# Optimization experiments

Hardware: AMD Instinct MI355X
Metric: run time of the kernel (lower is better)

## Reference

```python
import jax, jax.numpy as jnp
import numpy as np

B, N, C = 4, 2048, 768
H = 6  # 3 obj heads + 3 pose heads (forced by the chained matmul shapes)


def setup_inputs() -> dict:
    key = jax.random.key(0)
    k1, k2, k3 = jax.random.split(key, 3)
    x = jax.random.normal(k1, (B, N, C), dtype=jnp.float32)
    w_qkv = jax.random.normal(k2, (3 * C, C), dtype=jnp.float32) * (C ** -0.5)
    w_proj = jax.random.normal(k3, (C, C // 2), dtype=jnp.float32) * ((C // 2) ** -0.5)
    b_proj = jnp.zeros((C,), dtype=jnp.float32)
    return {"x": x, "w_qkv": w_qkv, "w_proj": w_proj, "b_proj": b_proj, "num_heads": H}


def reference(x, w_qkv, w_proj, b_proj, num_heads):
    b, n, c = x.shape
    hd = c // num_heads
    scale = hd ** -0.5
    # qkv projection -> [3, B, H, N, hd]
    qkv = (x @ w_qkv.T).reshape(b, n, 3, num_heads, hd)
    qkv = jnp.transpose(qkv, (2, 0, 3, 1, 4))
    q, k, v = qkv[0], qkv[1], qkv[2]
    # head split: first 3 heads -> obj (sigmoid), last 3 -> pose (softmax)
    attn_obj = jax.nn.sigmoid(jnp.einsum('bhqd,bhkd->bhqk', q[:, 0:3], k[:, 0:3]) * scale)
    attn_pose = jax.nn.softmax(jnp.einsum('bhqd,bhkd->bhqk', q[:, 3:], k[:, 3:]) * scale, axis=-1)
    # chained matmuls: (attn_pose @ (attn_obj @ v_pose))  -> [B, 3, N, hd]
    ctx = jnp.einsum('bhqk,bhkd->bhqd', attn_obj, v[:, 3:])
    ctx = jnp.einsum('bhqk,bhkd->bhqd', attn_pose, ctx)
    out = jnp.transpose(ctx, (0, 2, 1, 3)).reshape(b, n, c // 2)
    out = out @ w_proj.T + b_proj
    return out, attn_obj
```

## Files before the change

kernel.cpp:

```cpp
#include <hip/hip_runtime.h>

typedef _Float16 half8 __attribute__((ext_vector_type(8)));
typedef _Float16 half4v __attribute__((ext_vector_type(4)));
typedef float f32x4 __attribute__((ext_vector_type(4)));
typedef float f32x16 __attribute__((ext_vector_type(16)));

#define MFMA16(a, b, c) __builtin_amdgcn_mfma_f32_16x16x32_f16((a), (b), (c), 0, 0, 0)
#define MFMA32(a, b, c) __builtin_amdgcn_mfma_f32_32x32x16_f16((a), (b), (c), 0, 0, 0)
#define FENCE() __builtin_amdgcn_sched_barrier(0)
#define BAR() __builtin_amdgcn_s_barrier()

__device__ __forceinline__ void gl_lds16(const void* g, void* l) {
  __builtin_amdgcn_global_load_lds(
      (const __attribute__((address_space(1))) unsigned int*)g,
      (__attribute__((address_space(3))) unsigned int*)l, 16, 0, 0);
}

__device__ __forceinline__ unsigned pkh2(float a, float b) {
  unsigned lo = (unsigned)__builtin_bit_cast(unsigned short, (_Float16)a);
  unsigned hf = (unsigned)__builtin_bit_cast(unsigned short, (_Float16)b);
  return lo | (hf << 16);
}

__global__ __launch_bounds__(256) void k_cvt_all(const float* __restrict__ x,
                                                 const float* __restrict__ wq,
                                                 const float* __restrict__ wp,
                                                 _Float16* __restrict__ xb,
                                                 _Float16* __restrict__ wqb,
                                                 _Float16* __restrict__ wpb) {
  int i = blockIdx.x * 256 + threadIdx.x;
  const float4* src;
  half4v* dst;
  int j;
  if (i < 1572864) { src = (const float4*)x; dst = (half4v*)xb; j = i; }
  else if (i < 1572864 + 442368) { src = (const float4*)wq; dst = (half4v*)wqb; j = i - 1572864; }
  else if (i < 2088960) { src = (const float4*)wp; dst = (half4v*)wpb; j = i - 2015232; }
  else return;
  float4 v = src[j];
  half4v h;
  h[0] = (_Float16)v.x; h[1] = (_Float16)v.y;
  h[2] = (_Float16)v.z; h[3] = (_Float16)v.w;
  dst[j] = h;
}

__global__ __launch_bounds__(256) void k_qkv(const _Float16* __restrict__ A,
                                             const _Float16* __restrict__ Bt,
                                             _Float16* __restrict__ Qw,
                                             _Float16* __restrict__ Kw,
                                             _Float16* __restrict__ Vtw) {
  __shared__ _Float16 As[2][128 * 32];
  __shared__ _Float16 Bs[2][128 * 32];
  const int tid = threadIdx.x;
  const int w = tid >> 6, l = tid & 63;
  const int wr = w >> 1, wc = w & 1;
  const int bid0 = blockIdx.x;
  const int bid = (bid0 & 7) * 144 + (bid0 >> 3);
  const int tm = bid / 18, tn = bid % 18;
  const int m0 = tm * 128, n0 = tn * 128;

  auto stage = [&](int it, int dst) {
    int k0 = it * 32;
#pragma unroll
    for (int r = 0; r < 2; ++r) {
      int seg = r * 256 + tid;
      int row = seg >> 2, cs = seg & 3;
      gl_lds16(A + (size_t)(m0 + row) * 768 + k0 + cs * 8, (char*)As[dst] + (r * 256 + w * 64) * 16);
      gl_lds16(Bt + (size_t)(n0 + row) * 768 + k0 + cs * 8, (char*)Bs[dst] + (r * 256 + w * 64) * 16);
    }
  };

  f32x4 acc[4][4] = {};
  stage(0, 0);
  asm volatile("s_waitcnt vmcnt(0)" ::: "memory");
  BAR();
  for (int it = 0; it < 24; ++it) {
    const int cur = it & 1;
    stage(it < 23 ? it + 1 : 23, cur ^ 1);
    asm volatile("s_waitcnt vmcnt(4)" ::: "memory");
    FENCE();
    BAR();
    FENCE();
#pragma unroll
    for (int m = 0; m < 4; ++m) {
      half8 av = *(const half8*)&As[cur][(wr * 64 + m * 16 + (l & 15)) * 32 + (l >> 4) * 8];
#pragma unroll
      for (int n = 0; n < 4; ++n) {
        half8 bv = *(const half8*)&Bs[cur][(wc * 64 + n * 16 + (l & 15)) * 32 + (l >> 4) * 8];
        acc[m][n] = MFMA16(av, bv, acc[m][n]);
      }
    }
    FENCE();
    BAR();
  }
  asm volatile("s_waitcnt vmcnt(0)" ::: "memory");

  const float scale = 0.08838834764831845f;
#pragma unroll
  for (int m = 0; m < 4; ++m) {
    int gmb = m0 + wr * 64 + m * 16 + ((l >> 4) << 2);
#pragma unroll
    for (int n = 0; n < 4; ++n) {
      int gn0 = n0 + wc * 64 + n * 16;
      int t = gn0 / 768, rem = gn0 % 768;
      int h = rem >> 7, d = (rem & 127) + (l & 15);
      if (t == 2) {
        int bB = gmb >> 11, ntok0 = gmb & 2047;
        half4v hv;
#pragma unroll
        for (int j = 0; j < 4; ++j) hv[j] = (_Float16)acc[m][n][j];
        *(half4v*)&Vtw[((size_t)(bB * 6 + h) * 128 + d) * 2048 + ntok0] = hv;
      } else {
#pragma unroll
        for (int j = 0; j < 4; ++j) {
          int gm = gmb + j;
          int b = gm >> 11, ntok = gm & 2047;
          float v = acc[m][n][j];
          if (t == 0)
            Qw[((size_t)(b * 6 + h) * 2048 + ntok) * 128 + d] = (_Float16)(v * scale);
          else
            Kw[((size_t)(b * 6 + h) * 2048 + ntok) * 128 + d] = (_Float16)v;
        }
      }
    }
  }
}

__global__ __launch_bounds__(256, 3) void k_obj(const _Float16* __restrict__ Qw,
                                                const _Float16* __restrict__ Kw,
                                                const _Float16* __restrict__ Vtw,
                                                float* __restrict__ attn,
                                                float* __restrict__ c1p) {
  __shared__ _Float16 Ks[2][64 * 128];
  __shared__ _Float16 Vs[128 * 64];
  __shared__ float Ts[4][256];
  const int tid = threadIdx.x, w = tid >> 6, l = tid & 63;
  const int wr = w >> 1, wc = w & 1, hi = l >> 5, q = l & 31;
  const int bid0 = blockIdx.x;
  const int bid = (bid0 & 7) * 96 + (bid0 >> 3);
  const int kvh = bid & 1, u = bid >> 1;
  const int b = u / 96, remu = u % 96, h = remu / 32, qb = remu % 32;
  const int kvbase = kvh * 1024;
  const _Float16* Qg = Qw + ((size_t)(b * 6 + h) * 2048 + qb * 64 + wr * 32) * 128;
  const _Float16* Kg = Kw + ((size_t)(b * 6 + h) * 2048 + kvbase) * 128;
  const _Float16* Vg = Vtw + ((size_t)(b * 6 + h + 3) * 128) * 2048 + kvbase;
  float* attng = attn + ((size_t)(b * 3 + h) * 2048 + qb * 64) * 2048 + kvbase;
  float* c1g = c1p + ((size_t)(kvh * 12 + b * 3 + h) * 128) * 2048;

  auto stageK = [&](int t, int dstb) {
#pragma unroll
    for (int r = 0; r < 4; ++r) {
      int seg = r * 256 + tid;
      int row = seg >> 4, cs = (seg & 15) ^ (row & 7);
      gl_lds16(Kg + (size_t)(t * 64 + row) * 128 + cs * 8,
               (char*)Ks[dstb] + (r * 256 + w * 64) * 16);
    }
  };
  auto stageV = [&](int t) {
#pragma unroll
    for (int r = 0; r < 4; ++r) {
      int seg = r * 256 + tid;
      int row = seg >> 3, cs = (seg & 7) ^ (row & 7);
      gl_lds16(Vg + (size_t)row * 2048 + t * 64 + cs * 8,
               (char*)Vs + (r * 256 + w * 64) * 16);
    }
  };

  half8 qreg[8];
#pragma unroll
  for (int s = 0; s < 8; ++s)
    qreg[s] = *(const half8*)&Qg[(size_t)q * 128 + s * 16 + hi * 8];
  stageK(0, 0);

  f32x16 acc[4] = {};
  for (int kt = 0; kt < 16; ++kt) {
    const int cur = kt & 1, nxt = cur ^ 1;
    stageV(kt);
    stageK((kt + 1) & 15, nxt);
    asm volatile("s_waitcnt vmcnt(8)" ::: "memory");
    FENCE(); BAR(); FENCE();
    f32x16 p = {};
    const int krow = wc * 32 + q;
    __builtin_amdgcn_s_setprio(1);
#pragma unroll
    for (int s = 0; s < 8; ++s) {
      int chunk = (s * 2 + hi) ^ (krow & 7);
      half8 av = *(const half8*)&Ks[cur][krow * 128 + chunk * 8];
      p = MFMA32(av, qreg[s], p);
    }
    __builtin_amdgcn_s_setprio(0);
#pragma unroll
    for (int r = 0; r < 16; ++r) p[r] = 1.0f / (1.0f + __expf(-p[r]));
    union { unsigned uu[4]; half8 v; } bf0, bf1;
    {
      unsigned pk01 = pkh2(p[0], p[1]), pk23 = pkh2(p[2], p[3]);
      unsigned pk45 = pkh2(p[4], p[5]), pk67 = pkh2(p[6], p[7]);
      unsigned x = hi ? pk01 : pk45, y = hi ? pk23 : pk67;
      unsigned xsw = (unsigned)__shfl_xor((int)x, 32);
      unsigned ysw = (unsigned)__shfl_xor((int)y, 32);
      bf0.uu[0] = hi ? xsw : pk01; bf0.uu[1] = hi ? ysw : pk23;
      bf0.uu[2] = hi ? pk45 : xsw; bf0.uu[3] = hi ? pk67 : ysw;
    }
    {
      unsigned pk01 = pkh2(p[8], p[9]), pk23 = pkh2(p[10], p[11]);
      unsigned pk45 = pkh2(p[12], p[13]), pk67 = pkh2(p[14], p[15]);
      unsigned x = hi ? pk01 : pk45, y = hi ? pk23 : pk67;
      unsigned xsw = (unsigned)__shfl_xor((int)x, 32);
      unsigned ysw = (unsigned)__shfl_xor((int)y, 32);
      bf1.uu[0] = hi ? xsw : pk01; bf1.uu[1] = hi ? ysw : pk23;
      bf1.uu[2] = hi ? pk45 : xsw; bf1.uu[3] = hi ? pk67 : ysw;
    }
    asm volatile("s_waitcnt vmcnt(4)" ::: "memory");
    FENCE(); BAR(); FENCE();
    __builtin_amdgcn_s_setprio(1);
#pragma unroll
    for (int ks = 0; ks < 2; ++ks) {
#pragma unroll
      for (int dt = 0; dt < 4; ++dt) {
        int vrow = dt * 32 + q;
        int chunk = (wc * 4 + ks * 2 + hi) ^ (vrow & 7);
        half8 av = *(const half8*)&Vs[vrow * 64 + chunk * 8];
        acc[dt] = MFMA32(av, ks ? bf1.v : bf0.v, acc[dt]);
      }
    }
    __builtin_amdgcn_s_setprio(0);
#pragma unroll
    for (int rho = 0; rho < 4; ++rho) {
      asm volatile("s_waitcnt lgkmcnt(0)" ::: "memory");
      FENCE();
      if ((q >> 3) == rho) {
        int qr = q & 7;
#pragma unroll
        for (int g = 0; g < 4; ++g) {
          f32x4 vv;
          vv[0] = p[g * 4 + 0]; vv[1] = p[g * 4 + 1];
          vv[2] = p[g * 4 + 2]; vv[3] = p[g * 4 + 3];
          int kv0 = g * 8 + hi * 4;
          *(f32x4*)&Ts[w][qr * 32 + (kv0 ^ (qr << 2))] = vv;
        }
      }
      asm volatile("s_waitcnt lgkmcnt(0)" ::: "memory");
      FENCE();
      {
        int row = l >> 3, c0 = (l & 7) * 4;
        f32x4 vv = *(const f32x4*)&Ts[w][row * 32 + (c0 ^ (row << 2))];
        *(f32x4*)&attng[(size_t)(wr * 32 + rho * 8 + row) * 2048 + kt * 64 + wc * 32 + c0] = vv;
      }
    }
    FENCE();
    BAR();
  }
  __syncthreads();
  float* mb = (float*)Ks;
  if (wc == 1) {
#pragma unroll
    for (int dt = 0; dt < 4; ++dt)
#pragma unroll
      for (int r = 0; r < 16; ++r) {
        int d = dt * 32 + (r & 3) + 8 * (r >> 2) + 4 * hi;
        mb[(wr * 128 + d) * 32 + q] = acc[dt][r];
      }
  }
  __syncthreads();
  if (wc == 0) {
    int n = qb * 64 + wr * 32 + q;
#pragma unroll
    for (int dt = 0; dt < 4; ++dt)
#pragma unroll
      for (int r = 0; r < 16; ++r) {
        int d = dt * 32 + (r & 3) + 8 * (r >> 2) + 4 * hi;
        c1g[(size_t)d * 2048 + n] = acc[dt][r] + mb[(wr * 128 + d) * 32 + q];
      }
  }
}

__global__ __launch_bounds__(256) void k_merge1(const float* __restrict__ c1p,
                                                _Float16* __restrict__ c1t) {
  int i = blockIdx.x * 256 + threadIdx.x;
  f32x4 a = ((const f32x4*)c1p)[i];
  f32x4 bb = ((const f32x4*)c1p)[i + 786432];
  half4v hv;
#pragma unroll
  for (int j = 0; j < 4; ++j) hv[j] = (_Float16)(a[j] + bb[j]);
  ((half4v*)c1t)[i] = hv;
}

__global__ __launch_bounds__(256, 3) void k_pose(const _Float16* __restrict__ Qw,
                                                 const _Float16* __restrict__ Kw,
                                                 const _Float16* __restrict__ c1t,
                                                 float* __restrict__ p2,
                                                 float* __restrict__ lsumw) {
  __shared__ _Float16 Ks[2][64 * 128];
  __shared__ _Float16 Cs[128 * 64];
  __shared__ float lbuf[64];
  const int tid = threadIdx.x, w = tid >> 6, l = tid & 63;
  const int wr = w >> 1, wc = w & 1, hi = l >> 5, q = l & 31;
  const int bid0 = blockIdx.x;
  const int bid = (bid0 & 7) * 96 + (bid0 >> 3);
  const int kvh = bid & 1, u = bid >> 1;
  const int b = u / 96, remu = u % 96, h = remu / 32, qb = remu % 32;
  const int kvbase = kvh * 1024;
  const _Float16* Qg = Qw + ((size_t)(b * 6 + h + 3) * 2048 + qb * 64 + wr * 32) * 128;
  const _Float16* Kg = Kw + ((size_t)(b * 6 + h + 3) * 2048 + kvbase) * 128;
  const _Float16* Cg = c1t + ((size_t)(b * 3 + h) * 128) * 2048 + kvbase;
  float* p2g = p2 + (size_t)kvh * 3145728 + (size_t)b * 2048 * 384;

  auto stageK = [&](int t, int dstb) {
#pragma unroll
    for (int r = 0; r < 4; ++r) {
      int seg = r * 256 + tid;
      int row = seg >> 4, cs = (seg & 15) ^ (row & 7);
      gl_lds16(Kg + (size_t)(t * 64 + row) * 128 + cs * 8,
               (char*)Ks[dstb] + (r * 256 + w * 64) * 16);
    }
  };
  auto stageC = [&](int t) {
#pragma unroll
    for (int r = 0; r < 4; ++r) {
      int seg = r * 256 + tid;
      int row = seg >> 3, cs = (seg & 7) ^ (row & 7);
      gl_lds16(Cg + (size_t)row * 2048 + t * 64 + cs * 8,
               (char*)Cs + (r * 256 + w * 64) * 16);
    }
  };

  half8 qreg[8];
#pragma unroll
  for (int s = 0; s < 8; ++s)
    qreg[s] = *(const half8*)&Qg[(size_t)q * 128 + s * 16 + hi * 8];
  stageK(0, 0);

  f32x16 acc[4] = {};
  float lsum = 0.f;
  for (int kt = 0; kt < 16; ++kt) {
    const int cur = kt & 1, nxt = cur ^ 1;
    stageC(kt);
    stageK((kt + 1) & 15, nxt);
    asm volatile("s_waitcnt vmcnt(8)" ::: "memory");
    FENCE(); BAR(); FENCE();
    f32x16 p = {};
    const int krow = wc * 32 + q;
    __builtin_amdgcn_s_setprio(1);
#pragma unroll
    for (int s = 0; s < 8; ++s) {
      int chunk = (s * 2 + hi) ^ (krow & 7);
      half8 av = *(const half8*)&Ks[cur][krow * 128 + chunk * 8];
      p = MFMA32(av, qreg[s], p);
    }
    __builtin_amdgcn_s_setprio(0);
#pragma unroll
    for (int r = 0; r < 16; ++r) {
      p[r] = __expf(p[r]);
      lsum += p[r];
    }
    union { unsigned uu[4]; half8 v; } bf0, bf1;
    {
      unsigned pk01 = pkh2(p[0], p[1]), pk23 = pkh2(p[2], p[3]);
      unsigned pk45 = pkh2(p[4], p[5]), pk67 = pkh2(p[6], p[7]);
      unsigned x = hi ? pk01 : pk45, y = hi ? pk23 : pk67;
      unsigned xsw = (unsigned)__shfl_xor((int)x, 32);
      unsigned ysw = (unsigned)__shfl_xor((int)y, 32);
      bf0.uu[0] = hi ? xsw : pk01; bf0.uu[1] = hi ? ysw : pk23;
      bf0.uu[2] = hi ? pk45 : xsw; bf0.uu[3] = hi ? pk67 : ysw;
    }
    {
      unsigned pk01 = pkh2(p[8], p[9]), pk23 = pkh2(p[10], p[11]);
      unsigned pk45 = pkh2(p[12], p[13]), pk67 = pkh2(p[14], p[15]);
      unsigned x = hi ? pk01 : pk45, y = hi ? pk23 : pk67;
      unsigned xsw = (unsigned)__shfl_xor((int)x, 32);
      unsigned ysw = (unsigned)__shfl_xor((int)y, 32);
      bf1.uu[0] = hi ? xsw : pk01; bf1.uu[1] = hi ? ysw : pk23;
      bf1.uu[2] = hi ? pk45 : xsw; bf1.uu[3] = hi ? pk67 : ysw;
    }
    asm volatile("s_waitcnt vmcnt(4)" ::: "memory");
    FENCE(); BAR(); FENCE();
    __builtin_amdgcn_s_setprio(1);
#pragma unroll
    for (int ks = 0; ks < 2; ++ks) {
#pragma unroll
      for (int dt = 0; dt < 4; ++dt) {
        int vrow = dt * 32 + q;
        int chunk = (wc * 4 + ks * 2 + hi) ^ (vrow & 7);
        half8 av = *(const half8*)&Cs[vrow * 64 + chunk * 8];
        acc[dt] = MFMA32(av, ks ? bf1.v : bf0.v, acc[dt]);
      }
    }
    __builtin_amdgcn_s_setprio(0);
    FENCE();
    BAR();
  }
  __syncthreads();
  float lsum2 = lsum + (float)__shfl_xor(lsum, 32);
  float* mb = (float*)Ks;
  if (wc == 1) {
#pragma unroll
    for (int dt = 0; dt < 4; ++dt)
#pragma unroll
      for (int r = 0; r < 16; ++r) {
        int d = dt * 32 + (r & 3) + 8 * (r >> 2) + 4 * hi;
        mb[(wr * 128 + d) * 32 + q] = acc[dt][r];
      }
    if (hi == 0) lbuf[wr * 32 + q] = lsum2;
  }
  __syncthreads();
  float* Cf = (float*)Cs;
  if (wc == 0) {
#pragma unroll
    for (int dt = 0; dt < 4; ++dt)
#pragma unroll
      for (int r = 0; r < 16; ++r) {
        int d = dt * 32 + (r & 3) + 8 * (r >> 2) + 4 * hi;
        acc[dt][r] += mb[(wr * 128 + d) * 32 + q];
      }
    float lsump = lsum2 + lbuf[wr * 32 + q];
    if (hi == 0)
      lsumw[(size_t)(kvh * 12 + b * 3 + h) * 2048 + qb * 64 + wr * 32 + q] = lsump;
  }
#pragma unroll
  for (int rr = 0; rr < 2; ++rr) {
    __syncthreads();
    if (wc == 0 && wr == rr) {
#pragma unroll
      for (int dt = 0; dt < 4; ++dt)
#pragma unroll
        for (int g = 0; g < 4; ++g) {
          int d0 = dt * 32 + g * 8 + hi * 4, c = d0 >> 2;
          f32x4 vv;
          vv[0] = acc[dt][g * 4 + 0]; vv[1] = acc[dt][g * 4 + 1];
          vv[2] = acc[dt][g * 4 + 2]; vv[3] = acc[dt][g * 4 + 3];
          *(f32x4*)&Cf[q * 128 + ((c ^ ((q & 7) << 2)) << 2)] = vv;
        }
    }
    __syncthreads();
    {
      int nl = tid >> 3, cbase = (tid & 7) * 4;
#pragma unroll
      for (int j = 0; j < 4; ++j) {
        int c = cbase + j;
        f32x4 vv = *(const f32x4*)&Cf[nl * 128 + ((c ^ ((nl & 7) << 2)) << 2)];
        *(f32x4*)&p2g[(size_t)(qb * 64 + rr * 32 + nl) * 384 + h * 128 + (c << 2)] = vv;
      }
    }
  }
}

__global__ __launch_bounds__(256) void k_merge2(const float* __restrict__ p2,
                                                const float* __restrict__ lsumw,
                                                _Float16* __restrict__ c2) {
  int i = blockIdx.x * 256 + threadIdx.x;
  size_t i4 = (size_t)i * 4;
  int n = (int)(i4 / 384);
  int h = ((int)(i4 % 384)) >> 7;
  int b = n >> 11, nl = n & 2047;
  int hh = b * 3 + h;
  float ls = lsumw[hh * 2048 + nl] + lsumw[24576 + hh * 2048 + nl];
  float inv = 1.0f / ls;
  f32x4 a = ((const f32x4*)p2)[i];
  f32x4 bb = ((const f32x4*)p2)[i + 786432];
  half4v hv;
#pragma unroll
  for (int j = 0; j < 4; ++j) hv[j] = (_Float16)((a[j] + bb[j]) * inv);
  ((half4v*)c2)[i] = hv;
}

__global__ __launch_bounds__(256) void k_proj(const _Float16* __restrict__ A,
                                              const _Float16* __restrict__ Bt,
                                              const float* __restrict__ bias,
                                              float* __restrict__ out) {
  __shared__ _Float16 As[2][128 * 32];
  __shared__ _Float16 Bs[2][128 * 32];
  const int tid = threadIdx.x;
  const int w = tid >> 6, l = tid & 63;
  const int wr = w >> 1, wc = w & 1;
  const int bid0 = blockIdx.x;
  const int bid = (bid0 & 7) * 48 + (bid0 >> 3);
  const int tm = bid / 6, tn = bid % 6;
  const int m0 = tm * 128, n0 = tn * 128;

  auto stage = [&](int it, int dst) {
    int k0 = it * 32;
#pragma unroll
    for (int r = 0; r < 2; ++r) {
      int seg = r * 256 + tid;
      int row = seg >> 2, cs = seg & 3;
      gl_lds16(A + (size_t)(m0 + row) * 384 + k0 + cs * 8, (char*)As[dst] + (r * 256 + w * 64) * 16);
      gl_lds16(Bt + (size_t)(n0 + row) * 384 + k0 + cs * 8, (char*)Bs[dst] + (r * 256 + w * 64) * 16);
    }
  };

  f32x4 acc[4][4] = {};
  stage(0, 0);
  asm volatile("s_waitcnt vmcnt(0)" ::: "memory");
  BAR();
  for (int it = 0; it < 12; ++it) {
    const int cur = it & 1;
    stage(it < 11 ? it + 1 : 11, cur ^ 1);
    asm volatile("s_waitcnt vmcnt(4)" ::: "memory");
    FENCE();
    BAR();
    FENCE();
#pragma unroll
    for (int m = 0; m < 4; ++m) {
      half8 av = *(const half8*)&As[cur][(wr * 64 + m * 16 + (l & 15)) * 32 + (l >> 4) * 8];
#pragma unroll
      for (int n = 0; n < 4; ++n) {
        half8 bv = *(const half8*)&Bs[cur][(wc * 64 + n * 16 + (l & 15)) * 32 + (l >> 4) * 8];
        acc[m][n] = MFMA16(av, bv, acc[m][n]);
      }
    }
    FENCE();
    BAR();
  }
  asm volatile("s_waitcnt vmcnt(0)" ::: "memory");

#pragma unroll
  for (int m = 0; m < 4; ++m) {
    int gmb = m0 + wr * 64 + m * 16 + ((l >> 4) << 2);
#pragma unroll
    for (int n = 0; n < 4; ++n) {
      int gn = n0 + wc * 64 + n * 16 + (l & 15);
      float bv = bias[gn];
#pragma unroll
      for (int j = 0; j < 4; ++j) {
        int gm = gmb + j;
        out[(size_t)gm * 768 + gn] = acc[m][n][j] + bv;
      }
    }
  }
}

extern "C" void kernel_launch(void* const* d_in, const int* in_sizes, int n_in,
                              void* d_out, int out_size, void* d_ws, size_t ws_size,
                              hipStream_t stream) {
  const float* x = (const float*)d_in[0];
  const float* wqkv = (const float*)d_in[1];
  const float* wproj = (const float*)d_in[2];
  const float* bproj = (const float*)d_in[3];

  _Float16* xb = (_Float16*)d_ws;
  _Float16* wqkvb = xb + 6291456;
  _Float16* wprojb = wqkvb + 1769472;
  _Float16* Qw = wprojb + 294912;
  _Float16* Kw = Qw + 6291456;
  _Float16* Vtw = Kw + 6291456;
  _Float16* c1t = Vtw + 6291456;
  _Float16* c2 = c1t + 3145728;
  float* c1p = (float*)(c2 + 3145728);
  float* p2 = c1p + 6291456;
  float* lsumw = p2 + 6291456;

  float* out = (float*)d_out;
  float* attn = out + 6291456;

  k_cvt_all<<<8160, 256, 0, stream>>>(x, wqkv, wproj, xb, wqkvb, wprojb);
  k_qkv<<<1152, 256, 0, stream>>>(xb, wqkvb, Qw, Kw, Vtw);
  k_obj<<<768, 256, 0, stream>>>(Qw, Kw, Vtw, attn, c1p);
  k_merge1<<<3072, 256, 0, stream>>>(c1p, c1t);
  k_pose<<<768, 256, 0, stream>>>(Qw, Kw, c1t, p2, lsumw);
  k_merge2<<<3072, 256, 0, stream>>>(p2, lsumw, c2);
  k_proj<<<384, 256, 0, stream>>>(c2, wprojb, bproj, out);
}
```

Before: 216.7 us.

## Remove split-KV in obj/pose kernels and fuse merges into epilogues

The obj and pose attention kernels no longer split the key range into two halves. Each block now loops over all 2048 keys and writes the final fp16 context directly, normalised by the softmax sum in the pose case. This removes the two merge kernels and the fp32 partial buffers, along with their global traffic and launch cost. The attn tile store is reorganised to do a single LDS transpose per tile, and occupancy for k_obj drops to 2 blocks per CU. The trade-off is half as many blocks (384 on a 256-CU device), which risks poor load balance and less latency hiding.

```diff
diff --git a/kernel.cpp b/kernel.cpp
--- a/kernel.cpp
+++ b/kernel.cpp
@@ -125,26 +125,23 @@
   }
 }
 
-__global__ __launch_bounds__(256, 3) void k_obj(const _Float16* __restrict__ Qw,
+__global__ __launch_bounds__(256, 2) void k_obj(const _Float16* __restrict__ Qw,
                                                 const _Float16* __restrict__ Kw,
                                                 const _Float16* __restrict__ Vtw,
                                                 float* __restrict__ attn,
-                                                float* __restrict__ c1p) {
+                                                _Float16* __restrict__ c1t) {
   __shared__ _Float16 Ks[2][64 * 128];
   __shared__ _Float16 Vs[128 * 64];
-  __shared__ float Ts[4][256];
+  __shared__ float Ts[4][1024];
   const int tid = threadIdx.x, w = tid >> 6, l = tid & 63;
   const int wr = w >> 1, wc = w & 1, hi = l >> 5, q = l & 31;
   const int bid0 = blockIdx.x;
-  const int bid = (bid0 & 7) * 96 + (bid0 >> 3);
-  const int kvh = bid & 1, u = bid >> 1;
-  const int b = u / 96, remu = u % 96, h = remu / 32, qb = remu % 32;
-  const int kvbase = kvh * 1024;
+  const int bid = (bid0 & 7) * 48 + (bid0 >> 3);
+  const int b = bid / 96, rem = bid % 96, h = rem / 32, qb = rem % 32;
   const _Float16* Qg = Qw + ((size_t)(b * 6 + h) * 2048 + qb * 64 + wr * 32) * 128;
-  const _Float16* Kg = Kw + ((size_t)(b * 6 + h) * 2048 + kvbase) * 128;
-  const _Float16* Vg = Vtw + ((size_t)(b * 6 + h + 3) * 128) * 2048 + kvbase;
-  float* attng = attn + ((size_t)(b * 3 + h) * 2048 + qb * 64) * 2048 + kvbase;
-  float* c1g = c1p + ((size_t)(kvh * 12 + b * 3 + h) * 128) * 2048;
+  const _Float16* Kg = Kw + ((size_t)(b * 6 + h) * 2048) * 128;
+  const _Float16* Vg = Vtw + ((size_t)(b * 6 + h + 3) * 128) * 2048;
+  float* attng = attn + ((size_t)(b * 3 + h) * 2048 + qb * 64) * 2048;
 
   auto stageK = [&](int t, int dstb) {
 #pragma unroll
@@ -172,10 +169,10 @@
   stageK(0, 0);
 
   f32x16 acc[4] = {};
-  for (int kt = 0; kt < 16; ++kt) {
+  for (int kt = 0; kt < 32; ++kt) {
     const int cur = kt & 1, nxt = cur ^ 1;
     stageV(kt);
-    stageK((kt + 1) & 15, nxt);
+    stageK((kt + 1) & 31, nxt);
     asm volatile("s_waitcnt vmcnt(8)" ::: "memory");
     FENCE(); BAR(); FENCE();
     f32x16 p = {};
@@ -223,27 +220,19 @@
       }
     }
     __builtin_amdgcn_s_setprio(0);
-#pragma unroll
-    for (int rho = 0; rho < 4; ++rho) {
-      asm volatile("s_waitcnt lgkmcnt(0)" ::: "memory");
-      FENCE();
-      if ((q >> 3) == rho) {
-        int qr = q & 7;
-#pragma unroll
-        for (int g = 0; g < 4; ++g) {
-          f32x4 vv;
-          vv[0] = p[g * 4 + 0]; vv[1] = p[g * 4 + 1];
-          vv[2] = p[g * 4 + 2]; vv[3] = p[g * 4 + 3];
-          int kv0 = g * 8 + hi * 4;
-          *(f32x4*)&Ts[w][qr * 32 + (kv0 ^ (qr << 2))] = vv;
-        }
-      }
-      asm volatile("s_waitcnt lgkmcnt(0)" ::: "memory");
-      FENCE();
-      {
-        int row = l >> 3, c0 = (l & 7) * 4;
-        f32x4 vv = *(const f32x4*)&Ts[w][row * 32 + (c0 ^ (row << 2))];
-        *(f32x4*)&attng[(size_t)(wr * 32 + rho * 8 + row) * 2048 + kt * 64 + wc * 32 + c0] = vv;
+    {
+      float* T = Ts[w];
+#pragma unroll
+      for (int r = 0; r < 16; ++r) {
+        int kv = (r & 3) + 8 * (r >> 2) + 4 * hi;
+        T[q * 32 + (kv ^ ((q & 7) << 2))] = p[r];
+      }
+#pragma unroll
+      for (int i = 0; i < 4; ++i) {
+        int qr = (l >> 3) + 8 * i;
+        int kvq = (l & 7) * 4;
+        f32x4 v4 = *(const f32x4*)&T[qr * 32 + (kvq ^ ((qr & 7) << 2))];
+        *(f32x4*)&attng[(size_t)(wr * 32 + qr) * 2048 + kt * 64 + wc * 32 + kvq] = v4;
       }
     }
     FENCE();
@@ -262,47 +251,33 @@
   }
   __syncthreads();
   if (wc == 0) {
+    _Float16* cg = c1t + (size_t)(b * 3 + h) * 128 * 2048;
     int n = qb * 64 + wr * 32 + q;
 #pragma unroll
     for (int dt = 0; dt < 4; ++dt)
 #pragma unroll
       for (int r = 0; r < 16; ++r) {
         int d = dt * 32 + (r & 3) + 8 * (r >> 2) + 4 * hi;
-        c1g[(size_t)d * 2048 + n] = acc[dt][r] + mb[(wr * 128 + d) * 32 + q];
-      }
-  }
-}
-
-__global__ __launch_bounds__(256) void k_merge1(const float* __restrict__ c1p,
-                                                _Float16* __restrict__ c1t) {
-  int i = blockIdx.x * 256 + threadIdx.x;
-  f32x4 a = ((const f32x4*)c1p)[i];
-  f32x4 bb = ((const f32x4*)c1p)[i + 786432];
-  half4v hv;
-#pragma unroll
-  for (int j = 0; j < 4; ++j) hv[j] = (_Float16)(a[j] + bb[j]);
-  ((half4v*)c1t)[i] = hv;
+        cg[(size_t)d * 2048 + n] = (_Float16)(acc[dt][r] + mb[(wr * 128 + d) * 32 + q]);
+      }
+  }
 }
 
 __global__ __launch_bounds__(256, 3) void k_pose(const _Float16* __restrict__ Qw,
                                                  const _Float16* __restrict__ Kw,
                                                  const _Float16* __restrict__ c1t,
-                                                 float* __restrict__ p2,
-                                                 float* __restrict__ lsumw) {
+                                                 _Float16* __restrict__ c2) {
   __shared__ _Float16 Ks[2][64 * 128];
   __shared__ _Float16 Cs[128 * 64];
   __shared__ float lbuf[64];
   const int tid = threadIdx.x, w = tid >> 6, l = tid & 63;
   const int wr = w >> 1, wc = w & 1, hi = l >> 5, q = l & 31;
   const int bid0 = blockIdx.x;
-  const int bid = (bid0 & 7) * 96 + (bid0 >> 3);
-  const int kvh = bid & 1, u = bid >> 1;
-  const int b = u / 96, remu = u % 96, h = remu / 32, qb = remu % 32;
-  const int kvbase = kvh * 1024;
+  const int bid = (bid0 & 7) * 48 + (bid0 >> 3);
+  const int b = bid / 96, rem = bid % 96, h = rem / 32, qb = rem % 32;
   const _Float16* Qg = Qw + ((size_t)(b * 6 + h + 3) * 2048 + qb * 64 + wr * 32) * 128;
-  const _Float16* Kg = Kw + ((size_t)(b * 6 + h + 3) * 2048 + kvbase) * 128;
-  const _Float16* Cg = c1t + ((size_t)(b * 3 + h) * 128) * 2048 + kvbase;
-  float* p2g = p2 + (size_t)kvh * 3145728 + (size_t)b * 2048 * 384;
+  const _Float16* Kg = Kw + ((size_t)(b * 6 + h + 3) * 2048) * 128;
+  const _Float16* Cg = c1t + ((size_t)(b * 3 + h) * 128) * 2048;
 
   auto stageK = [&](int t, int dstb) {
 #pragma unroll
@@ -331,10 +306,10 @@
 
   f32x16 acc[4] = {};
   float lsum = 0.f;
-  for (int kt = 0; kt < 16; ++kt) {
+  for (int kt = 0; kt < 32; ++kt) {
     const int cur = kt & 1, nxt = cur ^ 1;
     stageC(kt);
-    stageK((kt + 1) & 15, nxt);
+    stageK((kt + 1) & 31, nxt);
     asm volatile("s_waitcnt vmcnt(8)" ::: "memory");
     FENCE(); BAR(); FENCE();
     f32x16 p = {};
@@ -391,6 +366,7 @@
   __syncthreads();
   float lsum2 = lsum + (float)__shfl_xor(lsum, 32);
   float* mb = (float*)Ks;
+  _Float16* ob = (_Float16*)Cs;
   if (wc == 1) {
 #pragma unroll
     for (int dt = 0; dt < 4; ++dt)
@@ -399,67 +375,40 @@
         int d = dt * 32 + (r & 3) + 8 * (r >> 2) + 4 * hi;
         mb[(wr * 128 + d) * 32 + q] = acc[dt][r];
       }
-    if (hi == 0) lbuf[wr * 32 + q] = lsum2;
+    if (l < 32) lbuf[wr * 32 + q] = lsum2;
   }
   __syncthreads();
-  float* Cf = (float*)Cs;
   if (wc == 0) {
+    float inv = 1.0f / (lsum2 + lbuf[wr * 32 + q]);
+    int qbl = wr * 32 + q;
 #pragma unroll
     for (int dt = 0; dt < 4; ++dt)
 #pragma unroll
-      for (int r = 0; r < 16; ++r) {
-        int d = dt * 32 + (r & 3) + 8 * (r >> 2) + 4 * hi;
-        acc[dt][r] += mb[(wr * 128 + d) * 32 + q];
-      }
-    float lsump = lsum2 + lbuf[wr * 32 + q];
-    if (hi == 0)
-      lsumw[(size_t)(kvh * 12 + b * 3 + h) * 2048 + qb * 64 + wr * 32 + q] = lsump;
-  }
-#pragma unroll
-  for (int rr = 0; rr < 2; ++rr) {
-    __syncthreads();
-    if (wc == 0 && wr == rr) {
-#pragma unroll
-      for (int dt = 0; dt < 4; ++dt)
-#pragma unroll
-        for (int g = 0; g < 4; ++g) {
-          int d0 = dt * 32 + g * 8 + hi * 4, c = d0 >> 2;
-          f32x4 vv;
-          vv[0] = acc[dt][g * 4 + 0]; vv[1] = acc[dt][g * 4 + 1];
-          vv[2] = acc[dt][g * 4 + 2]; vv[3] = acc[dt][g * 4 + 3];
-          *(f32x4*)&Cf[q * 128 + ((c ^ ((q & 7) << 2)) << 2)] = vv;
-        }
-    }
-    __syncthreads();
-    {
-      int nl = tid >> 3, cbase = (tid & 7) * 4;
-#pragma unroll
-      for (int j = 0; j < 4; ++j) {
-        int c = cbase + j;
-        f32x4 vv = *(const f32x4*)&Cf[nl * 128 + ((c ^ ((nl & 7) << 2)) << 2)];
-        *(f32x4*)&p2g[(size_t)(qb * 64 + rr * 32 + nl) * 384 + h * 128 + (c << 2)] = vv;
-      }
-    }
-  }
-}
-
-__global__ __launch_bounds__(256) void k_merge2(const float* __restrict__ p2,
-                                                const float* __restrict__ lsumw,
-                                                _Float16* __restrict__ c2) {
-  int i = blockIdx.x * 256 + threadIdx.x;
-  size_t i4 = (size_t)i * 4;
-  int n = (int)(i4 / 384);
-  int h = ((int)(i4 % 384)) >> 7;
-  int b = n >> 11, nl = n & 2047;
-  int hh = b * 3 + h;
-  float ls = lsumw[hh * 2048 + nl] + lsumw[24576 + hh * 2048 + nl];
-  float inv = 1.0f / ls;
-  f32x4 a = ((const f32x4*)p2)[i];
-  f32x4 bb = ((const f32x4*)p2)[i + 786432];
-  half4v hv;
-#pragma unroll
-  for (int j = 0; j < 4; ++j) hv[j] = (_Float16)((a[j] + bb[j]) * inv);
-  ((half4v*)c2)[i] = hv;
+      for (int g = 0; g < 4; ++g) {
+        int d0 = dt * 32 + 8 * g + 4 * hi;
+        float v0 = (acc[dt][4 * g + 0] + mb[(wr * 128 + d0 + 0) * 32 + q]) * inv;
+        float v1 = (acc[dt][4 * g + 1] + mb[(wr * 128 + d0 + 1) * 32 + q]) * inv;
+        float v2 = (acc[dt][4 * g + 2] + mb[(wr * 128 + d0 + 2) * 32 + q]) * inv;
+        float v3 = (acc[dt][4 * g + 3] + mb[(wr * 128 + d0 + 3) * 32 + q]) * inv;
+        union { unsigned u[2]; half4v v; } hv;
+        hv.u[0] = pkh2(v0, v1);
+        hv.u[1] = pkh2(v2, v3);
+        int c8 = (d0 >> 2) ^ ((qbl & 7) << 2);
+        *(half4v*)&ob[qbl * 128 + c8 * 4] = hv.v;
+      }
+  }
+  __syncthreads();
+  {
+    _Float16* cg = c2 + ((size_t)b * 2048 + qb * 64) * 384 + h * 128;
+    int qbl = tid >> 2;
+#pragma unroll
+    for (int j = 0; j < 4; ++j) {
+      int ii = (tid & 3) + j * 4;
+      int c8 = (ii * 2) ^ ((qbl & 7) << 2);
+      half8 v = *(const half8*)&ob[qbl * 128 + c8 * 4];
+      *(half8*)&cg[(size_t)qbl * 384 + ii * 8] = v;
+    }
+  }
 }
 
 __global__ __launch_bounds__(256) void k_proj(const _Float16* __restrict__ A,
@@ -544,18 +493,13 @@
   _Float16* Vtw = Kw + 6291456;
   _Float16* c1t = Vtw + 6291456;
   _Float16* c2 = c1t + 3145728;
-  float* c1p = (float*)(c2 + 3145728);
-  float* p2 = c1p + 6291456;
-  float* lsumw = p2 + 6291456;
 
   float* out = (float*)d_out;
   float* attn = out + 6291456;
 
   k_cvt_all<<<8160, 256, 0, stream>>>(x, wqkv, wproj, xb, wqkvb, wprojb);
   k_qkv<<<1152, 256, 0, stream>>>(xb, wqkvb, Qw, Kw, Vtw);
-  k_obj<<<768, 256, 0, stream>>>(Qw, Kw, Vtw, attn, c1p);
-  k_merge1<<<3072, 256, 0, stream>>>(c1p, c1t);
-  k_pose<<<768, 256, 0, stream>>>(Qw, Kw, c1t, p2, lsumw);
-  k_merge2<<<3072, 256, 0, stream>>>(p2, lsumw, c2);
+  k_obj<<<384, 256, 0, stream>>>(Qw, Kw, Vtw, attn, c1t);
+  k_pose<<<384, 256, 0, stream>>>(Qw, Kw, c1t, c2);
   k_proj<<<384, 256, 0, stream>>>(c2, wprojb, bproj, out);
 }
```

New measurement: 216.1 us. About the same (-0.3%).
